# Kernel optimization log

Hardware: AMD Instinct MI355X
Metric: run time of the kernel (lower is better)

The kernel has to match this reference:

```python
import jax, jax.numpy as jnp
import numpy as np

B, D_IN, UNITS, KFEAT = 2048, 2048, 1024, 49


def setup_inputs() -> dict:
    key = jax.random.key(0)
    ks = jax.random.split(key, 10)
    s = 0.02  # small init scale to keep sigmoids/tanh unsaturated
    return {
        "inputs": jax.random.normal(ks[0], (B, D_IN), jnp.float32),
        "h_tm": jax.random.normal(ks[1], (B, UNITS), jnp.float32),
        "m_tm": jax.random.normal(ks[2], (B, UNITS), jnp.float32),
        "v_seq": jax.random.normal(ks[3], (B, KFEAT, UNITS), jnp.float32),
        # gate weights stacked along output dim in order [f, i, o, g, a]
        "W_gates": jax.random.normal(ks[4], (UNITS, 5 * UNITS), jnp.float32) * s,
        "U_gates": jax.random.normal(ks[5], (D_IN, 5 * UNITS), jnp.float32) * s,
        "b_gates": jnp.zeros((5 * UNITS,), jnp.float32),
        "W_z": jax.random.normal(ks[6], (UNITS, KFEAT + 1), jnp.float32) * s,
        "U_z": jax.random.normal(ks[7], (UNITS, KFEAT + 1), jnp.float32) * s,
        "W_h": jax.random.normal(ks[8], (KFEAT + 1, 1), jnp.float32) * s,
    }


def reference(inputs, h_tm, m_tm, v_seq, W_gates, U_gates, b_gates, W_z, U_z, W_h):
    U = h_tm.shape[-1]
    # fused gate pre-activations: [B, 5U]
    z = h_tm @ W_gates + inputs @ U_gates + b_gates
    f, i, o, g, a = (z[:, j * U:(j + 1) * U] for j in range(5))
    ft = jax.nn.sigmoid(f)
    it = jax.nn.sigmoid(i)
    ot = jax.nn.sigmoid(o)
    gt = jax.nn.sigmoid(g)
    at = jnp.tanh(a)
    mt = m_tm * ft + it * at               # memory cell
    tanh_mt = jnp.tanh(mt)
    ht = ot * tanh_mt                      # hidden state
    st = gt * tanh_mt                      # visual sentinel
    # sentinel-augmented features: [B, K+1, U]
    v_expand = jnp.concatenate([v_seq, st[:, None, :]], axis=1)
    vtt = jnp.einsum('bku,uz->bkz', v_expand, W_z)   # [B, K+1, K+1]
    dtt = (ht @ U_z)[:, None, :]                     # broadcast over K+1 (K.repeat)
    zt = jnp.einsum('bkz,zo->bko', jnp.tanh(vtt + dtt), W_h)  # [B, K+1, 1]
    # NOTE: original uses keras softmax with default axis=-1 on a size-1 axis
    alpha_t = jax.nn.softmax(zt, axis=-1)            # [B, K+1, 1]
    ct = jnp.sum(alpha_t * v_expand, axis=1)         # batch_dot(axes=1) + squeeze
    return (ht + ct, ht, mt)
```

## Files before the change

### kernel.cpp

```cpp
#include <hip/hip_runtime.h>
#include <stdint.h>

#define BB   2048
#define DIN  2048
#define UU   1024
#define KF   49
#define GM   2048
#define GK   3072
#define GN   5120

#define BM    128
#define UC    64
#define BROWS 320
#define BKS   32
#define NST   96
#define BUFB  28672

typedef __bf16  bf16x8 __attribute__((ext_vector_type(8)));
typedef float   f32x4  __attribute__((ext_vector_type(4)));

static __device__ __forceinline__ unsigned short f2bf(float f) {
    union { float f; unsigned u; } x; x.f = f;
    unsigned u = x.u;
    unsigned r = (u + 0x7fffu + ((u >> 16) & 1u)) >> 16;
    return (unsigned short)r;
}

__global__ void prep(const float* __restrict__ h, const float* __restrict__ x,
                     const float* __restrict__ Wg, const float* __restrict__ Ug,
                     unsigned short* __restrict__ A, unsigned short* __restrict__ Wt) {
    __shared__ float t[32][36];
    if (blockIdx.x < 6144) {
        int idx = blockIdx.x * 256 + threadIdx.x;
        int b = idx / (GK / 4);
        int k = (idx % (GK / 4)) * 4;
        float4 v;
        if (k < UU) v = *(const float4*)(h + (size_t)b * UU + k);
        else        v = *(const float4*)(x + (size_t)b * DIN + (k - UU));
        ushort4 o;
        o.x = f2bf(v.x); o.y = f2bf(v.y); o.z = f2bf(v.z); o.w = f2bf(v.w);
        *(ushort4*)(A + (size_t)idx * 4) = o;
    } else {
        int bid2 = blockIdx.x - 6144;
        int k0 = (bid2 % (GK / 32)) * 32;
        int n0 = (bid2 / (GK / 32)) * 32;
        int r  = threadIdx.x >> 3;
        int cq = threadIdx.x & 7;
        int k = k0 + r;
        const float* src = (k < UU) ? (Wg + (size_t)k * GN) : (Ug + (size_t)(k - UU) * GN);
        *(float4*)&t[r][cq * 4] = *(const float4*)(src + n0 + cq * 4);
        __syncthreads();
        int n = n0 + r;
        int u = n & (UU - 1);
        int g = n >> 10;
        ushort4 o;
        o.x = f2bf(t[cq * 4 + 0][r]);
        o.y = f2bf(t[cq * 4 + 1][r]);
        o.z = f2bf(t[cq * 4 + 2][r]);
        o.w = f2bf(t[cq * 4 + 3][r]);
        *(ushort4*)(Wt + (size_t)(u * 5 + g) * GK + k0 + cq * 4) = o;
    }
}

__global__ __launch_bounds__(512, 2) void gemm_fused(
        const unsigned short* __restrict__ A, const unsigned short* __restrict__ Wt,
        const float* __restrict__ m_tm, const float* __restrict__ bg,
        const float* __restrict__ v_seq, float* __restrict__ out) {
    __shared__ __align__(16) char lds[2 * 28672];

    const int tid  = threadIdx.x;
    const int lane = tid & 63;
    const int wave = tid >> 6;
    const int wr = wave >> 2;
    const int wc = wave & 3;
    const int brow  = blockIdx.y * BM;
    const int ucol0 = blockIdx.x * UC;

    f32x4 acc[4][5];
#pragma unroll
    for (int m = 0; m < 4; m++)
#pragma unroll
        for (int g = 0; g < 5; g++) acc[m][g] = (f32x4){0.f, 0.f, 0.f, 0.f};

    const unsigned short* src[4];
    int ldsoff[4];
#pragma unroll
    for (int t = 0; t < 4; t++) {
        int j = t * 512 + tid;
        if (j < 512) {
            src[t] = A + (size_t)(brow + (j >> 2)) * GK + (j & 3) * 8;
            ldsoff[t] = j * 16;
        } else {
            int jj = j - 512;
            if (jj > 1279) jj = 1279;
            src[t] = Wt + (size_t)((size_t)ucol0 * 5 + (jj >> 2)) * GK + (jj & 3) * 8;
            ldsoff[t] = 8192 + jj * 16;
        }
    }

    const int aoff = (wr * 64 + (lane & 15)) * 64 + (lane >> 4) * 16;
    const int boff = 8192 + ((wc * 16 + (lane & 15)) * 5) * 64 + (lane >> 4) * 16;

    auto STAGE = [&](int kstep, int bufbase) {
        const int koff = kstep * BKS;
#pragma unroll
        for (int t = 0; t < 3; t++)
            __builtin_amdgcn_global_load_lds(
                (const __attribute__((address_space(1))) void*)(src[t] + koff),
                (__attribute__((address_space(3))) void*)(lds + bufbase + ldsoff[t]), 16, 0, 0);
        if (tid < 256)
            __builtin_amdgcn_global_load_lds(
                (const __attribute__((address_space(1))) void*)(src[3] + koff),
                (__attribute__((address_space(3))) void*)(lds + bufbase + ldsoff[3]), 16, 0, 0);
    };

    auto COMPUTE = [&](int bufbase) {
        bf16x8 af[4], bfr[5];
#pragma unroll
        for (int m = 0; m < 4; m++) af[m]  = *(const bf16x8*)(lds + bufbase + aoff + m * 1024);
#pragma unroll
        for (int g = 0; g < 5; g++) bfr[g] = *(const bf16x8*)(lds + bufbase + boff + g * 64);
#pragma unroll
        for (int m = 0; m < 4; m++)
#pragma unroll
            for (int g = 0; g < 5; g++)
                acc[m][g] = __builtin_amdgcn_mfma_f32_16x16x32_bf16(af[m], bfr[g], acc[m][g], 0, 0, 0);
    };

    const float* vp = v_seq + (size_t)(brow + (tid >> 4)) * (KF * UU) + ucol0 + (tid & 15) * 4;
    const size_t RG = (size_t)32 * KF * UU;
    float4 vacc0 = {0,0,0,0}, vacc1 = {0,0,0,0}, vacc2 = {0,0,0,0}, vacc3 = {0,0,0,0};

    STAGE(0, 0);
    __syncthreads();

    for (int tp = 0; tp < 48; ++tp) {
        {
            STAGE(2 * tp + 1, BUFB);
            const float4 v0 = *(const float4*)(vp + (size_t)tp * UU);
            const float4 v1 = *(const float4*)(vp + RG + (size_t)tp * UU);
            COMPUTE(0);
            vacc0.x += v0.x; vacc0.y += v0.y; vacc0.z += v0.z; vacc0.w += v0.w;
            vacc1.x += v1.x; vacc1.y += v1.y; vacc1.z += v1.z; vacc1.w += v1.w;
            __syncthreads();
        }
        {
            if (tp < 47) STAGE(2 * tp + 2, 0);
            const float4 v2 = *(const float4*)(vp + 2 * RG + (size_t)tp * UU);
            const float4 v3 = *(const float4*)(vp + 3 * RG + (size_t)tp * UU);
            COMPUTE(BUFB);
            vacc2.x += v2.x; vacc2.y += v2.y; vacc2.z += v2.z; vacc2.w += v2.w;
            vacc3.x += v3.x; vacc3.y += v3.y; vacc3.z += v3.z; vacc3.w += v3.w;
            __syncthreads();
        }
    }

    {
        const float4 w0 = *(const float4*)(vp + (size_t)48 * UU);
        const float4 w1 = *(const float4*)(vp + RG + (size_t)48 * UU);
        const float4 w2 = *(const float4*)(vp + 2 * RG + (size_t)48 * UU);
        const float4 w3 = *(const float4*)(vp + 3 * RG + (size_t)48 * UU);
        vacc0.x += w0.x; vacc0.y += w0.y; vacc0.z += w0.z; vacc0.w += w0.w;
        vacc1.x += w1.x; vacc1.y += w1.y; vacc1.z += w1.z; vacc1.w += w1.w;
        vacc2.x += w2.x; vacc2.y += w2.y; vacc2.z += w2.z; vacc2.w += w2.w;
        vacc3.x += w3.x; vacc3.y += w3.y; vacc3.z += w3.z; vacc3.w += w3.w;
    }

    float* lv = (float*)lds;
    {
        const int xr = tid >> 4, xc = (tid & 15) * 4;
        *(float4*)&lv[(size_t)(xr +  0) * 68 + xc] = vacc0;
        *(float4*)&lv[(size_t)(xr + 32) * 68 + xc] = vacc1;
        *(float4*)&lv[(size_t)(xr + 64) * 68 + xc] = vacc2;
        *(float4*)&lv[(size_t)(xr + 96) * 68 + xc] = vacc3;
    }
    __syncthreads();

    const int ucol = ucol0 + wc * 16 + (lane & 15);
    const int lcol = wc * 16 + (lane & 15);
    const float b0 = bg[0 * UU + ucol];
    const float b1 = bg[1 * UU + ucol];
    const float b2 = bg[2 * UU + ucol];
    const float b3 = bg[3 * UU + ucol];
    const float b4 = bg[4 * UU + ucol];
    const int lr0 = wr * 64 + ((lane >> 4) << 2);
    float* out0 = out;
    float* out1 = out + (size_t)GM * UU;
    float* out2 = out + 2 * (size_t)GM * UU;
#pragma unroll
    for (int m = 0; m < 4; m++) {
#pragma unroll
        for (int j = 0; j < 4; j++) {
            const int lrow = lr0 + m * 16 + j;
            const int row  = brow + lrow;
            const size_t idx = (size_t)row * UU + ucol;
            const float vs  = lv[(size_t)lrow * 68 + lcol];
            const float mtm = m_tm[idx];
            const float f = acc[m][0][j] + b0;
            const float i = acc[m][1][j] + b1;
            const float o = acc[m][2][j] + b2;
            const float g = acc[m][3][j] + b3;
            const float a = acc[m][4][j] + b4;
            const float ft = 1.f / (1.f + __expf(-f));
            const float it = 1.f / (1.f + __expf(-i));
            const float ot = 1.f / (1.f + __expf(-o));
            const float gt = 1.f / (1.f + __expf(-g));
            const float at = tanhf(a);
            const float mtv = mtm * ft + it * at;
            const float tm  = tanhf(mtv);
            const float ht  = ot * tm;
            const float st  = gt * tm;
            out0[idx] = ht + vs + st;
            out1[idx] = ht;
            out2[idx] = mtv;
        }
    }
}

extern "C" void kernel_launch(void* const* d_in, const int* in_sizes, int n_in,
                              void* d_out, int out_size, void* d_ws, size_t ws_size,
                              hipStream_t stream) {
    (void)in_sizes; (void)n_in; (void)out_size; (void)ws_size;
    const float* inputs  = (const float*)d_in[0];
    const float* h_tm    = (const float*)d_in[1];
    const float* m_tm    = (const float*)d_in[2];
    const float* v_seq   = (const float*)d_in[3];
    const float* W_gates = (const float*)d_in[4];
    const float* U_gates = (const float*)d_in[5];
    const float* b_gates = (const float*)d_in[6];

    char* ws = (char*)d_ws;
    unsigned short* Abf = (unsigned short*)ws;
    unsigned short* Wt  = (unsigned short*)(ws + 12582912);
    float* out = (float*)d_out;

    hipLaunchKernelGGL(prep, dim3(6144 + (GK / 32) * (GN / 32)), dim3(256), 0, stream,
                       h_tm, inputs, W_gates, U_gates, Abf, Wt);
    hipLaunchKernelGGL(gemm_fused, dim3(UU / UC, GM / BM), dim3(512), 0, stream,
                       Abf, Wt, m_tm, b_gates, v_seq, out);
}
```

Baseline: 194.9 us.

## Prefetch v_seq one step ahead with inline-asm loads and explicit vmcnt waits

The v_seq row-sum loads are now issued through inline-asm global_load_dwordx4 one pipeline step ahead of their use and are consumed in the next half-iteration. Each __syncthreads is replaced by an explicit s_waitcnt vmcnt(2) plus s_barrier and a sched_barrier, so the barrier only waits for the LDS staging loads and not for the in-flight v_seq prefetches. The last iteration is peeled so no out-of-range tile is staged. The goal is to hide the latency of the large v_seq stream behind the MFMA work. The cost is fragile hand-managed vmcnt accounting that depends on how many loads STAGE issues, and the compiler can no longer reorder around the barriers.

```diff
diff --git a/kernel.cpp b/kernel.cpp
--- a/kernel.cpp
+++ b/kernel.cpp
@@ -11,13 +11,15 @@
 
 #define BM    128
 #define UC    64
-#define BROWS 320
 #define BKS   32
 #define NST   96
-#define BUFB  28672
+#define SZBUF 28672
 
 typedef __bf16  bf16x8 __attribute__((ext_vector_type(8)));
 typedef float   f32x4  __attribute__((ext_vector_type(4)));
+
+#define VL(dst, ptr) asm volatile("global_load_dwordx4 %0, %1, off" \
+                                  : "=v"(dst) : "v"(ptr) : "memory")
 
 static __device__ __forceinline__ unsigned short f2bf(float f) {
     union { float f; unsigned u; } x; x.f = f;
@@ -66,7 +68,7 @@
         const unsigned short* __restrict__ A, const unsigned short* __restrict__ Wt,
         const float* __restrict__ m_tm, const float* __restrict__ bg,
         const float* __restrict__ v_seq, float* __restrict__ out) {
-    __shared__ __align__(16) char lds[2 * 28672];
+    __shared__ __align__(16) char lds[2 * SZBUF];
 
     const int tid  = threadIdx.x;
     const int lane = tid & 63;
@@ -129,31 +131,49 @@
 
     const float* vp = v_seq + (size_t)(brow + (tid >> 4)) * (KF * UU) + ucol0 + (tid & 15) * 4;
     const size_t RG = (size_t)32 * KF * UU;
-    float4 vacc0 = {0,0,0,0}, vacc1 = {0,0,0,0}, vacc2 = {0,0,0,0}, vacc3 = {0,0,0,0};
-
+    f32x4 vacc0 = {0,0,0,0}, vacc1 = {0,0,0,0}, vacc2 = {0,0,0,0}, vacc3 = {0,0,0,0};
+    f32x4 slA0, slA1, slB0, slB1;
+
+    VL(slA0, vp);
+    VL(slA1, vp + RG);
+    VL(slB0, vp + 2 * RG);
+    VL(slB1, vp + 3 * RG);
     STAGE(0, 0);
+    asm volatile("s_waitcnt vmcnt(0)" ::: "memory");
+    __builtin_amdgcn_s_barrier();
+    __builtin_amdgcn_sched_barrier(0);
+
+    for (int tp = 0; tp < 47; ++tp) {
+        {
+            vacc0 += slA0; vacc1 += slA1;
+            STAGE(2 * tp + 1, SZBUF);
+            VL(slA0, vp + (size_t)(tp + 1) * UU);
+            VL(slA1, vp + RG + (size_t)(tp + 1) * UU);
+            COMPUTE(0);
+            asm volatile("s_waitcnt vmcnt(2)" ::: "memory");
+            __builtin_amdgcn_s_barrier();
+            __builtin_amdgcn_sched_barrier(0);
+        }
+        {
+            vacc2 += slB0; vacc3 += slB1;
+            STAGE(2 * tp + 2, 0);
+            VL(slB0, vp + 2 * RG + (size_t)(tp + 1) * UU);
+            VL(slB1, vp + 3 * RG + (size_t)(tp + 1) * UU);
+            COMPUTE(SZBUF);
+            asm volatile("s_waitcnt vmcnt(2)" ::: "memory");
+            __builtin_amdgcn_s_barrier();
+            __builtin_amdgcn_sched_barrier(0);
+        }
+    }
+    vacc0 += slA0; vacc1 += slA1;
+    STAGE(95, SZBUF);
+    COMPUTE(0);
+    asm volatile("s_waitcnt vmcnt(0)" ::: "memory");
+    __builtin_amdgcn_s_barrier();
+    __builtin_amdgcn_sched_barrier(0);
+    vacc2 += slB0; vacc3 += slB1;
+    COMPUTE(SZBUF);
     __syncthreads();
-
-    for (int tp = 0; tp < 48; ++tp) {
-        {
-            STAGE(2 * tp + 1, BUFB);
-            const float4 v0 = *(const float4*)(vp + (size_t)tp * UU);
-            const float4 v1 = *(const float4*)(vp + RG + (size_t)tp * UU);
-            COMPUTE(0);
-            vacc0.x += v0.x; vacc0.y += v0.y; vacc0.z += v0.z; vacc0.w += v0.w;
-            vacc1.x += v1.x; vacc1.y += v1.y; vacc1.z += v1.z; vacc1.w += v1.w;
-            __syncthreads();
-        }
-        {
-            if (tp < 47) STAGE(2 * tp + 2, 0);
-            const float4 v2 = *(const float4*)(vp + 2 * RG + (size_t)tp * UU);
-            const float4 v3 = *(const float4*)(vp + 3 * RG + (size_t)tp * UU);
-            COMPUTE(BUFB);
-            vacc2.x += v2.x; vacc2.y += v2.y; vacc2.z += v2.z; vacc2.w += v2.w;
-            vacc3.x += v3.x; vacc3.y += v3.y; vacc3.z += v3.z; vacc3.w += v3.w;
-            __syncthreads();
-        }
-    }
 
     {
         const float4 w0 = *(const float4*)(vp + (size_t)48 * UU);
@@ -169,10 +189,10 @@
     float* lv = (float*)lds;
     {
         const int xr = tid >> 4, xc = (tid & 15) * 4;
-        *(float4*)&lv[(size_t)(xr +  0) * 68 + xc] = vacc0;
-        *(float4*)&lv[(size_t)(xr + 32) * 68 + xc] = vacc1;
-        *(float4*)&lv[(size_t)(xr + 64) * 68 + xc] = vacc2;
-        *(float4*)&lv[(size_t)(xr + 96) * 68 + xc] = vacc3;
+        *(f32x4*)&lv[(size_t)(xr +  0) * 68 + xc] = vacc0;
+        *(f32x4*)&lv[(size_t)(xr + 32) * 68 + xc] = vacc1;
+        *(f32x4*)&lv[(size_t)(xr + 64) * 68 + xc] = vacc2;
+        *(f32x4*)&lv[(size_t)(xr + 96) * 68 + xc] = vacc3;
     }
     __syncthreads();
 
```

New measurement: 182.2 us. 6.5% less time.

## Pre-swizzle bf16 operands into MFMA fragment order and load directly to registers

Applied to the files above, without the earlier changes.

The prep kernel now writes A and the transposed weights in a layout that matches the per-lane MFMA fragment order, tiled by row block and k-step. The GEMM drops LDS staging and barriers and instead loads fragments straight from global memory into double-buffered registers, prefetching the next k-step while computing the current one. The aim is to remove LDS traffic and per-step __syncthreads. In exchange, each wave re-reads operands that waves sharing a tile would otherwise share through LDS, which raises L2 and global traffic and register pressure.

```diff
diff --git a/kernel.cpp b/kernel.cpp
--- a/kernel.cpp
+++ b/kernel.cpp
@@ -11,13 +11,10 @@
 
 #define BM    128
 #define UC    64
-#define BROWS 320
-#define BKS   32
-#define NST   96
-#define BUFB  28672
 
 typedef __bf16  bf16x8 __attribute__((ext_vector_type(8)));
 typedef float   f32x4  __attribute__((ext_vector_type(4)));
+typedef unsigned short u16x8 __attribute__((ext_vector_type(8)));
 
 static __device__ __forceinline__ unsigned short f2bf(float f) {
     union { float f; unsigned u; } x; x.f = f;
@@ -30,20 +27,27 @@
                      const float* __restrict__ Wg, const float* __restrict__ Ug,
                      unsigned short* __restrict__ A, unsigned short* __restrict__ Wt) {
     __shared__ float t[32][36];
-    if (blockIdx.x < 6144) {
-        int idx = blockIdx.x * 256 + threadIdx.x;
-        int b = idx / (GK / 4);
-        int k = (idx % (GK / 4)) * 4;
-        float4 v;
-        if (k < UU) v = *(const float4*)(h + (size_t)b * UU + k);
-        else        v = *(const float4*)(x + (size_t)b * DIN + (k - UU));
-        ushort4 o;
-        o.x = f2bf(v.x); o.y = f2bf(v.y); o.z = f2bf(v.z); o.w = f2bf(v.w);
-        *(ushort4*)(A + (size_t)idx * 4) = o;
+    if (blockIdx.x < 3072) {
+        int cid = blockIdx.x * 256 + threadIdx.x;
+        int rb  = cid / 49152;
+        int rem = cid - rb * 49152;
+        int ts  = rem >> 9;
+        int j   = rem & 511;
+        int s = j >> 6, q = (j >> 4) & 3, r = j & 15;
+        int row = rb * 128 + s * 16 + r;
+        int k   = ts * 32 + q * 8;
+        const float* srcp = (k < UU) ? (h + (size_t)row * UU + k)
+                                     : (x + (size_t)row * DIN + (k - UU));
+        float4 lo = *(const float4*)(srcp);
+        float4 hi = *(const float4*)(srcp + 4);
+        u16x8 o;
+        o[0] = f2bf(lo.x); o[1] = f2bf(lo.y); o[2] = f2bf(lo.z); o[3] = f2bf(lo.w);
+        o[4] = f2bf(hi.x); o[5] = f2bf(hi.y); o[6] = f2bf(hi.z); o[7] = f2bf(hi.w);
+        *(u16x8*)(A + (size_t)cid * 8) = o;
     } else {
-        int bid2 = blockIdx.x - 6144;
-        int k0 = (bid2 % (GK / 32)) * 32;
-        int n0 = (bid2 / (GK / 32)) * 32;
+        int bid2 = blockIdx.x - 3072;
+        int k0 = (bid2 % 96) * 32;
+        int n0 = (bid2 / 96) * 32;
         int r  = threadIdx.x >> 3;
         int cq = threadIdx.x & 7;
         int k = k0 + r;
@@ -51,14 +55,20 @@
         *(float4*)&t[r][cq * 4] = *(const float4*)(src + n0 + cq * 4);
         __syncthreads();
         int n = n0 + r;
+        int g = n >> 10;
         int u = n & (UU - 1);
-        int g = n >> 10;
+        int cb = u >> 6, c = (u >> 4) & 3, rr = u & 15;
+        int tstep = k0 >> 5;
+        int q = cq >> 1, half = cq & 1;
+        int jch = (c * 5 + g) * 64 + q * 16 + rr;
+        size_t off = (size_t)cb * (96 * 1280 * 8) + (size_t)tstep * (1280 * 8)
+                   + (size_t)jch * 8 + half * 4;
         ushort4 o;
         o.x = f2bf(t[cq * 4 + 0][r]);
         o.y = f2bf(t[cq * 4 + 1][r]);
         o.z = f2bf(t[cq * 4 + 2][r]);
         o.w = f2bf(t[cq * 4 + 3][r]);
-        *(ushort4*)(Wt + (size_t)(u * 5 + g) * GK + k0 + cq * 4) = o;
+        *(ushort4*)(Wt + off) = o;
     }
 }
 
@@ -66,7 +76,7 @@
         const unsigned short* __restrict__ A, const unsigned short* __restrict__ Wt,
         const float* __restrict__ m_tm, const float* __restrict__ bg,
         const float* __restrict__ v_seq, float* __restrict__ out) {
-    __shared__ __align__(16) char lds[2 * 28672];
+    __shared__ float lv[128 * 68];
 
     const int tid  = threadIdx.x;
     const int lane = tid & 63;
@@ -82,107 +92,91 @@
 #pragma unroll
         for (int g = 0; g < 5; g++) acc[m][g] = (f32x4){0.f, 0.f, 0.f, 0.f};
 
-    const unsigned short* src[4];
-    int ldsoff[4];
-#pragma unroll
-    for (int t = 0; t < 4; t++) {
-        int j = t * 512 + tid;
-        if (j < 512) {
-            src[t] = A + (size_t)(brow + (j >> 2)) * GK + (j & 3) * 8;
-            ldsoff[t] = j * 16;
-        } else {
-            int jj = j - 512;
-            if (jj > 1279) jj = 1279;
-            src[t] = Wt + (size_t)((size_t)ucol0 * 5 + (jj >> 2)) * GK + (jj & 3) * 8;
-            ldsoff[t] = 8192 + jj * 16;
-        }
-    }
-
-    const int aoff = (wr * 64 + (lane & 15)) * 64 + (lane >> 4) * 16;
-    const int boff = 8192 + ((wc * 16 + (lane & 15)) * 5) * 64 + (lane >> 4) * 16;
-
-    auto STAGE = [&](int kstep, int bufbase) {
-        const int koff = kstep * BKS;
-#pragma unroll
-        for (int t = 0; t < 3; t++)
-            __builtin_amdgcn_global_load_lds(
-                (const __attribute__((address_space(1))) void*)(src[t] + koff),
-                (__attribute__((address_space(3))) void*)(lds + bufbase + ldsoff[t]), 16, 0, 0);
-        if (tid < 256)
-            __builtin_amdgcn_global_load_lds(
-                (const __attribute__((address_space(1))) void*)(src[3] + koff),
-                (__attribute__((address_space(3))) void*)(lds + bufbase + ldsoff[3]), 16, 0, 0);
-    };
-
-    auto COMPUTE = [&](int bufbase) {
-        bf16x8 af[4], bfr[5];
-#pragma unroll
-        for (int m = 0; m < 4; m++) af[m]  = *(const bf16x8*)(lds + bufbase + aoff + m * 1024);
-#pragma unroll
-        for (int g = 0; g < 5; g++) bfr[g] = *(const bf16x8*)(lds + bufbase + boff + g * 64);
-#pragma unroll
-        for (int m = 0; m < 4; m++)
-#pragma unroll
-            for (int g = 0; g < 5; g++)
-                acc[m][g] = __builtin_amdgcn_mfma_f32_16x16x32_bf16(af[m], bfr[g], acc[m][g], 0, 0, 0);
-    };
+    const char* pA = (const char*)A + ((size_t)blockIdx.y * (96 * 512)
+                                       + (size_t)(wr * 4) * 64 + lane) * 16;
+    const char* pB = (const char*)Wt + ((size_t)blockIdx.x * (96 * 1280)
+                                        + (size_t)(wc * 5) * 64 + lane) * 16;
 
     const float* vp = v_seq + (size_t)(brow + (tid >> 4)) * (KF * UU) + ucol0 + (tid & 15) * 4;
     const size_t RG = (size_t)32 * KF * UU;
-    float4 vacc0 = {0,0,0,0}, vacc1 = {0,0,0,0}, vacc2 = {0,0,0,0}, vacc3 = {0,0,0,0};
-
-    STAGE(0, 0);
-    __syncthreads();
-
+    f32x4 vacc0 = {0,0,0,0}, vacc1 = {0,0,0,0}, vacc2 = {0,0,0,0}, vacc3 = {0,0,0,0};
+
+    bf16x8 a0[4], b0[5], a1[4], b1[5];
+    f32x4 slA0, slA1, slB0, slB1;
+
+#pragma unroll
+    for (int m = 0; m < 4; m++) a0[m] = *(const bf16x8*)(pA + m * 1024);
+#pragma unroll
+    for (int g = 0; g < 5; g++) b0[g] = *(const bf16x8*)(pB + g * 1024);
+    slA0 = *(const f32x4*)(vp);
+    slA1 = *(const f32x4*)(vp + RG);
+    slB0 = *(const f32x4*)(vp + 2 * RG);
+    slB1 = *(const f32x4*)(vp + 3 * RG);
+
+    size_t ao = 8192, bo = 20480;
     for (int tp = 0; tp < 48; ++tp) {
         {
-            STAGE(2 * tp + 1, BUFB);
-            const float4 v0 = *(const float4*)(vp + (size_t)tp * UU);
-            const float4 v1 = *(const float4*)(vp + RG + (size_t)tp * UU);
-            COMPUTE(0);
-            vacc0.x += v0.x; vacc0.y += v0.y; vacc0.z += v0.z; vacc0.w += v0.w;
-            vacc1.x += v1.x; vacc1.y += v1.y; vacc1.z += v1.z; vacc1.w += v1.w;
-            __syncthreads();
+#pragma unroll
+            for (int m = 0; m < 4; m++) a1[m] = *(const bf16x8*)(pA + ao + m * 1024);
+#pragma unroll
+            for (int g = 0; g < 5; g++) b1[g] = *(const bf16x8*)(pB + bo + g * 1024);
+            vacc0 += slA0; vacc1 += slA1;
+            if (tp < 47) {
+                slA0 = *(const f32x4*)(vp + (size_t)(tp + 1) * UU);
+                slA1 = *(const f32x4*)(vp + RG + (size_t)(tp + 1) * UU);
+            }
+#pragma unroll
+            for (int m = 0; m < 4; m++)
+#pragma unroll
+                for (int g = 0; g < 5; g++)
+                    acc[m][g] = __builtin_amdgcn_mfma_f32_16x16x32_bf16(a0[m], b0[g], acc[m][g], 0, 0, 0);
+            ao += 8192; bo += 20480;
         }
         {
-            if (tp < 47) STAGE(2 * tp + 2, 0);
-            const float4 v2 = *(const float4*)(vp + 2 * RG + (size_t)tp * UU);
-            const float4 v3 = *(const float4*)(vp + 3 * RG + (size_t)tp * UU);
-            COMPUTE(BUFB);
-            vacc2.x += v2.x; vacc2.y += v2.y; vacc2.z += v2.z; vacc2.w += v2.w;
-            vacc3.x += v3.x; vacc3.y += v3.y; vacc3.z += v3.z; vacc3.w += v3.w;
-            __syncthreads();
+            if (tp < 47) {
+#pragma unroll
+                for (int m = 0; m < 4; m++) a0[m] = *(const bf16x8*)(pA + ao + m * 1024);
+#pragma unroll
+                for (int g = 0; g < 5; g++) b0[g] = *(const bf16x8*)(pB + bo + g * 1024);
+            }
+            vacc2 += slB0; vacc3 += slB1;
+            if (tp < 47) {
+                slB0 = *(const f32x4*)(vp + 2 * RG + (size_t)(tp + 1) * UU);
+                slB1 = *(const f32x4*)(vp + 3 * RG + (size_t)(tp + 1) * UU);
+            }
+#pragma unroll
+            for (int m = 0; m < 4; m++)
+#pragma unroll
+                for (int g = 0; g < 5; g++)
+                    acc[m][g] = __builtin_amdgcn_mfma_f32_16x16x32_bf16(a1[m], b1[g], acc[m][g], 0, 0, 0);
+            ao += 8192; bo += 20480;
         }
     }
 
     {
-        const float4 w0 = *(const float4*)(vp + (size_t)48 * UU);
-        const float4 w1 = *(const float4*)(vp + RG + (size_t)48 * UU);
-        const float4 w2 = *(const float4*)(vp + 2 * RG + (size_t)48 * UU);
-        const float4 w3 = *(const float4*)(vp + 3 * RG + (size_t)48 * UU);
-        vacc0.x += w0.x; vacc0.y += w0.y; vacc0.z += w0.z; vacc0.w += w0.w;
-        vacc1.x += w1.x; vacc1.y += w1.y; vacc1.z += w1.z; vacc1.w += w1.w;
-        vacc2.x += w2.x; vacc2.y += w2.y; vacc2.z += w2.z; vacc2.w += w2.w;
-        vacc3.x += w3.x; vacc3.y += w3.y; vacc3.z += w3.z; vacc3.w += w3.w;
-    }
-
-    float* lv = (float*)lds;
+        const f32x4 w0 = *(const f32x4*)(vp + (size_t)48 * UU);
+        const f32x4 w1 = *(const f32x4*)(vp + RG + (size_t)48 * UU);
+        const f32x4 w2 = *(const f32x4*)(vp + 2 * RG + (size_t)48 * UU);
+        const f32x4 w3 = *(const f32x4*)(vp + 3 * RG + (size_t)48 * UU);
+        vacc0 += w0; vacc1 += w1; vacc2 += w2; vacc3 += w3;
+    }
+
     {
         const int xr = tid >> 4, xc = (tid & 15) * 4;
-        *(float4*)&lv[(size_t)(xr +  0) * 68 + xc] = vacc0;
-        *(float4*)&lv[(size_t)(xr + 32) * 68 + xc] = vacc1;
-        *(float4*)&lv[(size_t)(xr + 64) * 68 + xc] = vacc2;
-        *(float4*)&lv[(size_t)(xr + 96) * 68 + xc] = vacc3;
+        *(f32x4*)&lv[(size_t)(xr +  0) * 68 + xc] = vacc0;
+        *(f32x4*)&lv[(size_t)(xr + 32) * 68 + xc] = vacc1;
+        *(f32x4*)&lv[(size_t)(xr + 64) * 68 + xc] = vacc2;
+        *(f32x4*)&lv[(size_t)(xr + 96) * 68 + xc] = vacc3;
     }
     __syncthreads();
 
     const int ucol = ucol0 + wc * 16 + (lane & 15);
     const int lcol = wc * 16 + (lane & 15);
-    const float b0 = bg[0 * UU + ucol];
-    const float b1 = bg[1 * UU + ucol];
-    const float b2 = bg[2 * UU + ucol];
-    const float b3 = bg[3 * UU + ucol];
-    const float b4 = bg[4 * UU + ucol];
+    const float c0 = bg[0 * UU + ucol];
+    const float c1 = bg[1 * UU + ucol];
+    const float c2 = bg[2 * UU + ucol];
+    const float c3 = bg[3 * UU + ucol];
+    const float c4 = bg[4 * UU + ucol];
     const int lr0 = wr * 64 + ((lane >> 4) << 2);
     float* out0 = out;
     float* out1 = out + (size_t)GM * UU;
@@ -196,11 +190,11 @@
             const size_t idx = (size_t)row * UU + ucol;
             const float vs  = lv[(size_t)lrow * 68 + lcol];
             const float mtm = m_tm[idx];
-            const float f = acc[m][0][j] + b0;
-            const float i = acc[m][1][j] + b1;
-            const float o = acc[m][2][j] + b2;
-            const float g = acc[m][3][j] + b3;
-            const float a = acc[m][4][j] + b4;
+            const float f = acc[m][0][j] + c0;
+            const float i = acc[m][1][j] + c1;
+            const float o = acc[m][2][j] + c2;
+            const float g = acc[m][3][j] + c3;
+            const float a = acc[m][4][j] + c4;
             const float ft = 1.f / (1.f + __expf(-f));
             const float it = 1.f / (1.f + __expf(-i));
             const float ot = 1.f / (1.f + __expf(-o));
@@ -234,7 +228,7 @@
     unsigned short* Wt  = (unsigned short*)(ws + 12582912);
     float* out = (float*)d_out;
 
-    hipLaunchKernelGGL(prep, dim3(6144 + (GK / 32) * (GN / 32)), dim3(256), 0, stream,
+    hipLaunchKernelGGL(prep, dim3(3072 + 96 * (GN / 32)), dim3(256), 0, stream,
                        h_tm, inputs, W_gates, U_gates, Abf, Wt);
     hipLaunchKernelGGL(gemm_fused, dim3(UU / UC, GM / BM), dim3(512), 0, stream,
                        Abf, Wt, m_tm, b_gates, v_seq, out);
```

After: 188.4 us. 3.3% less time.
